# Kernel tuning notes

Hardware: AMD Instinct MI355X
Metric: run time of the kernel (lower is better)

## Reference

```python
import jax, jax.numpy as jnp
import numpy as np

HIDDEN = 1024
NUM_EXPERTS = 64
MIN_K, MAX_K = 1, 4
THRESHOLD = 0.5
N_TOKENS = 32768


def setup_inputs() -> dict:
    key = jax.random.key(0)
    ks = jax.random.split(key, 6)
    std = 0.02
    h4 = HIDDEN // 4
    return {
        "hidden_states": jax.random.normal(ks[0], (N_TOKENS, HIDDEN), dtype=jnp.float32),
        "router_w": std * jax.random.normal(ks[1], (NUM_EXPERTS, HIDDEN), dtype=jnp.float32),
        "w1": std * jax.random.normal(ks[2], (h4, HIDDEN), dtype=jnp.float32),
        "b1": jnp.zeros((h4,), dtype=jnp.float32),
        "w2": std * jax.random.normal(ks[3], (1, h4), dtype=jnp.float32),
        "b2": jnp.zeros((1,), dtype=jnp.float32),
    }


def reference(hidden_states, router_w, w1, b1, w2, b2):
    # complexity predictor: Linear -> ReLU -> Linear -> Sigmoid, squeeze(-1)
    h = jax.nn.relu(hidden_states @ w1.T + b1)                     # [N, H/4]
    complexity = jax.nn.sigmoid(h @ w2.T + b2)[:, 0]               # [N]
    router_logits = hidden_states @ router_w.T                     # [N, E]

    adaptive_k = jnp.where(complexity > THRESHOLD, MAX_K, MIN_K)   # [N] int

    # vectorized adaptive top-k: take MAX_K everywhere, mask beyond k
    top_vals, top_idx = jax.lax.top_k(router_logits, MAX_K)        # [N, MAX_K]
    pos_mask = jnp.arange(MAX_K)[None, :] < adaptive_k[:, None]    # [N, MAX_K]
    masked_vals = jnp.where(pos_mask, top_vals, -jnp.inf)
    expert_weights = jax.nn.softmax(masked_vals, axis=-1)
    expert_weights = jnp.where(pos_mask, expert_weights, 0.0)      # zeros past k
    selected_experts = jnp.where(pos_mask, top_idx, 0)             # zeros past k

    # routing statistics
    probs = jax.nn.softmax(router_logits, axis=-1)                 # [N, E]
    expert_load = probs.mean(axis=0)                               # [E]
    load_variance = expert_load.var(ddof=1)                        # torch .var() is unbiased
    entropy = -(probs * jnp.log(probs + 1e-8)).sum(axis=-1).mean()

    return router_logits, selected_experts, expert_weights, load_variance, entropy
```

## Files before the change

### kernel.cpp

```cpp
#include <hip/hip_runtime.h>
#include <hip/hip_bf16.h>
#include <math.h>

#define NTOK 32768
#define HID  1024
#define NEXP 64
#define H4   256

typedef __attribute__((ext_vector_type(8))) short bf16x8;
typedef __attribute__((ext_vector_type(4))) float f32x4;

static __device__ __forceinline__ ushort f2bf(float x) {
    unsigned u = __float_as_uint(x);
    unsigned r = (u + 0x7FFFu + ((u >> 16) & 1u)) >> 16;
    return (ushort)r;
}

static __device__ __forceinline__ void split3r(float x, ushort &h, ushort &m, ushort &l) {
    h = f2bf(x);
    const float r1 = x - __uint_as_float(((unsigned)h) << 16);
    m = f2bf(r1);
    const float r2 = r1 - __uint_as_float(((unsigned)m) << 16);
    l = f2bf(r2);
}

#define SWZ(row, us) ((us) ^ (((row) & 7) << 3))

__global__ __launch_bounds__(256) void prep_kernel(
    const float* __restrict__ W1, const float* __restrict__ RW,
    ushort* __restrict__ W1h, ushort* __restrict__ W1l,
    ushort* __restrict__ RWh, ushort* __restrict__ RWm, ushort* __restrict__ RWl)
{
    if (blockIdx.x < 256) {
        const int id = blockIdx.x * 256 + threadIdx.x;
        const int c  = id >> 8;
        const int k0 = (id & 255) * 4;
        const float4 v = *(const float4*)(W1 + (size_t)c * HID + k0);
        const int p  = k0 >> 5;
        const int kk = k0 & 31;
        const size_t dst = (size_t)p * 8192 + (size_t)SWZ(c, c * 32 + kk);
        const float xs[4] = {v.x, v.y, v.z, v.w};
        ushort hv[4], lv[4];
#pragma unroll
        for (int j = 0; j < 4; j++) {
            const ushort h = f2bf(xs[j]);
            hv[j] = h;
            lv[j] = f2bf(xs[j] - __uint_as_float(((unsigned)h) << 16));
        }
        *(ushort4*)(W1h + dst) = make_ushort4(hv[0], hv[1], hv[2], hv[3]);
        *(ushort4*)(W1l + dst) = make_ushort4(lv[0], lv[1], lv[2], lv[3]);
    } else {
        const int e  = blockIdx.x - 256;
        const int k0 = threadIdx.x * 4;
        const float4 v = *(const float4*)(RW + (size_t)e * HID + k0);
        const float xs[4] = {v.x, v.y, v.z, v.w};
        ushort h[4], m[4], l[4];
#pragma unroll
        for (int j = 0; j < 4; j++) split3r(xs[j], h[j], m[j], l[j]);
        const int p  = k0 >> 5;
        const int kk = k0 & 31;
        const size_t dst = (size_t)p * 2048 + (size_t)SWZ(e, e * 32 + kk);
        *(ushort4*)(RWh + dst) = make_ushort4(h[0], h[1], h[2], h[3]);
        *(ushort4*)(RWm + dst) = make_ushort4(m[0], m[1], m[2], m[3]);
        *(ushort4*)(RWl + dst) = make_ushort4(l[0], l[1], l[2], l[3]);
    }
}

__global__ __launch_bounds__(512, 4) void fused_mfma(
    const float* __restrict__ X,
    const ushort* __restrict__ RWh, const ushort* __restrict__ RWm,
    const ushort* __restrict__ RWl,
    const ushort* __restrict__ W1h, const ushort* __restrict__ W1l,
    const float* __restrict__ B1, const float* __restrict__ W2,
    float* __restrict__ logits, float* __restrict__ s2ws)
{
    __shared__ __align__(16) ushort Xh[2048], Xm[2048], Xl[2048];
    __shared__ __align__(16) ushort RBh[2048], RBm[2048], RBl[2048];
    __shared__ __align__(16) ushort Wh[8192], Wl[8192];
    __shared__ float red[4][64];

    const int tid  = threadIdx.x;
    const int lane = tid & 63;
    const int w    = tid >> 6;
    const int quad = lane >> 4, l15 = lane & 15;
    const int tok0 = blockIdx.x * 64;
    const int rp   = w >> 2;
    const int cg   = w & 3;

    const int xrow = tid >> 3;
    const int xoff = (tid & 7) * 4;

    f32x4 accL[2];
    f32x4 accP[2][4];
#pragma unroll
    for (int f = 0; f < 2; f++) {
        accL[f] = (f32x4){0.f, 0.f, 0.f, 0.f};
#pragma unroll
        for (int j = 0; j < 4; j++) accP[f][j] = (f32x4){0.f, 0.f, 0.f, 0.f};
    }

    float w2r[4], b1r[4];
#pragma unroll
    for (int j = 0; j < 4; j++) {
        const int col = (cg * 4 + j) * 16 + l15;
        w2r[j] = W2[col];
        b1r[j] = B1[col];
    }

    const float* __restrict__ xsrc = X + (size_t)(tok0 + xrow) * HID + xoff;
    float4 xv = *(const float4*)(xsrc);

    for (int p = 0; p < 32; ++p) {
        {
            const float xs[4] = {xv.x, xv.y, xv.z, xv.w};
            ushort hv[4], mv[4], lv[4];
#pragma unroll
            for (int j = 0; j < 4; j++) split3r(xs[j], hv[j], mv[j], lv[j]);
            const int us = SWZ(xrow, xrow * 32 + xoff);
            *(ushort4*)&Xh[us] = make_ushort4(hv[0], hv[1], hv[2], hv[3]);
            *(ushort4*)&Xm[us] = make_ushort4(mv[0], mv[1], mv[2], mv[3]);
            *(ushort4*)&Xl[us] = make_ushort4(lv[0], lv[1], lv[2], lv[3]);
        }
        {
            const size_t pb = (size_t)p * 8192;
            __builtin_amdgcn_global_load_lds(
                (const __attribute__((address_space(1))) void*)(W1h + pb + (size_t)tid * 8),
                (__attribute__((address_space(3))) void*)((char*)Wh + (size_t)tid * 16), 16, 0, 0);
            __builtin_amdgcn_global_load_lds(
                (const __attribute__((address_space(1))) void*)(W1h + pb + (size_t)(tid + 512) * 8),
                (__attribute__((address_space(3))) void*)((char*)Wh + (size_t)(tid + 512) * 16), 16, 0, 0);
            __builtin_amdgcn_global_load_lds(
                (const __attribute__((address_space(1))) void*)(W1l + pb + (size_t)tid * 8),
                (__attribute__((address_space(3))) void*)((char*)Wl + (size_t)tid * 16), 16, 0, 0);
            __builtin_amdgcn_global_load_lds(
                (const __attribute__((address_space(1))) void*)(W1l + pb + (size_t)(tid + 512) * 8),
                (__attribute__((address_space(3))) void*)((char*)Wl + (size_t)(tid + 512) * 16), 16, 0, 0);
        }
        {
            const size_t pb = (size_t)p * 2048;
            if (tid < 256) {
                __builtin_amdgcn_global_load_lds(
                    (const __attribute__((address_space(1))) void*)(RWh + pb + (size_t)tid * 8),
                    (__attribute__((address_space(3))) void*)((char*)RBh + (size_t)tid * 16), 16, 0, 0);
                __builtin_amdgcn_global_load_lds(
                    (const __attribute__((address_space(1))) void*)(RWl + pb + (size_t)tid * 8),
                    (__attribute__((address_space(3))) void*)((char*)RBl + (size_t)tid * 16), 16, 0, 0);
            } else {
                const int i2 = tid - 256;
                __builtin_amdgcn_global_load_lds(
                    (const __attribute__((address_space(1))) void*)(RWm + pb + (size_t)i2 * 8),
                    (__attribute__((address_space(3))) void*)((char*)RBm + (size_t)i2 * 16), 16, 0, 0);
            }
        }
        __syncthreads();

        xv = *(const float4*)(xsrc + ((p + 1) & 31) * 32);

        bf16x8 axh[2], axm[2], axl[2];
#pragma unroll
        for (int f = 0; f < 2; ++f) {
            const int ra = rp * 32 + f * 16 + l15;
            const int ua = SWZ(ra, ra * 32 + quad * 8);
            axh[f] = *(const bf16x8*)&Xh[ua];
            axm[f] = *(const bf16x8*)&Xm[ua];
            axl[f] = *(const bf16x8*)&Xl[ua];
        }

        {
            const int rb = cg * 16 + l15;
            const int ub = SWZ(rb, rb * 32 + quad * 8);
            const bf16x8 rbh = *(const bf16x8*)&RBh[ub];
            const bf16x8 rbm = *(const bf16x8*)&RBm[ub];
            const bf16x8 rbl = *(const bf16x8*)&RBl[ub];
#pragma unroll
            for (int f = 0; f < 2; ++f) {
                accL[f] = __builtin_amdgcn_mfma_f32_16x16x32_bf16(axh[f], rbh, accL[f], 0, 0, 0);
                accL[f] = __builtin_amdgcn_mfma_f32_16x16x32_bf16(axm[f], rbh, accL[f], 0, 0, 0);
                accL[f] = __builtin_amdgcn_mfma_f32_16x16x32_bf16(axh[f], rbm, accL[f], 0, 0, 0);
                accL[f] = __builtin_amdgcn_mfma_f32_16x16x32_bf16(axl[f], rbh, accL[f], 0, 0, 0);
                accL[f] = __builtin_amdgcn_mfma_f32_16x16x32_bf16(axh[f], rbl, accL[f], 0, 0, 0);
                accL[f] = __builtin_amdgcn_mfma_f32_16x16x32_bf16(axm[f], rbm, accL[f], 0, 0, 0);
            }
        }

#pragma unroll
        for (int j = 0; j < 4; ++j) {
            const int rw = (cg * 4 + j) * 16 + l15;
            const int uw = SWZ(rw, rw * 32 + quad * 8);
            const bf16x8 bwh = *(const bf16x8*)&Wh[uw];
            const bf16x8 bwl = *(const bf16x8*)&Wl[uw];
#pragma unroll
            for (int f = 0; f < 2; ++f) {
                accP[f][j] = __builtin_amdgcn_mfma_f32_16x16x32_bf16(axh[f], bwh, accP[f][j], 0, 0, 0);
                accP[f][j] = __builtin_amdgcn_mfma_f32_16x16x32_bf16(axm[f], bwh, accP[f][j], 0, 0, 0);
                accP[f][j] = __builtin_amdgcn_mfma_f32_16x16x32_bf16(axh[f], bwl, accP[f][j], 0, 0, 0);
            }
        }
        __syncthreads();
    }

#pragma unroll
    for (int f = 0; f < 2; ++f)
#pragma unroll
        for (int r = 0; r < 4; ++r)
            logits[(size_t)(tok0 + (rp * 2 + f) * 16 + quad * 4 + r) * NEXP
                   + cg * 16 + l15] = accL[f][r];

#pragma unroll
    for (int f = 0; f < 2; ++f) {
#pragma unroll
        for (int r = 0; r < 4; ++r) {
            float s = 0.f;
#pragma unroll
            for (int j = 0; j < 4; ++j) {
                const float hval = accP[f][j][r] + b1r[j];
                s = fmaf(w2r[j], fmaxf(hval, 0.f), s);
            }
            s += __shfl_xor(s, 1);
            s += __shfl_xor(s, 2);
            s += __shfl_xor(s, 4);
            s += __shfl_xor(s, 8);
            if (l15 == 0)
                red[cg][rp * 32 + f * 16 + quad * 4 + r] = s;
        }
    }
    __syncthreads();
    if (tid < 64)
        s2ws[tok0 + tid] = red[0][tid] + red[1][tid] + red[2][tid] + red[3][tid];
}

__global__ __launch_bounds__(64) void route_kernel(
    const float* __restrict__ logits, const float* __restrict__ s2ws,
    const float* __restrict__ B2, float* __restrict__ sel,
    float* __restrict__ wts, float* __restrict__ load_sum,
    float* __restrict__ ent_sum)
{
    const int lane = threadIdx.x;
    const int tok  = blockIdx.x * 64 + lane;

    float r[64];
    const float* lr = logits + (size_t)tok * NEXP;
#pragma unroll
    for (int e4 = 0; e4 < 16; e4++) {
        float4 v = *(const float4*)(lr + e4 * 4);
        r[e4 * 4 + 0] = v.x; r[e4 * 4 + 1] = v.y;
        r[e4 * 4 + 2] = v.z; r[e4 * 4 + 3] = v.w;
    }

    float v0 = -1e30f, v1 = -1e30f, v2 = -1e30f, v3 = -1e30f;
    int   i0 = 0, i1 = 0, i2 = 0, i3 = 0;
#pragma unroll
    for (int e = 0; e < 64; e++) {
        const float v = r[e];
        if (v > v3) {
            if (v > v2) {
                if (v > v1) {
                    if (v > v0) { v3=v2;i3=i2; v2=v1;i2=i1; v1=v0;i1=i0; v0=v;i0=e; }
                    else        { v3=v2;i3=i2; v2=v1;i2=i1; v1=v;i1=e; }
                } else          { v3=v2;i3=i2; v2=v;i2=e; }
            } else              { v3=v;i3=e; }
        }
    }

    const float s2 = s2ws[tok] + B2[0];
    const bool k4 = (s2 > 0.f);

    float w0, w1v, w2v, w3v;
    int   s1i, s2i, s3i;
    if (k4) {
        const float e0 = expf(v0 - v0), e1 = expf(v1 - v0);
        const float e2 = expf(v2 - v0), e3 = expf(v3 - v0);
        const float inv4 = 1.f / (e0 + e1 + e2 + e3);
        w0 = e0 * inv4; w1v = e1 * inv4; w2v = e2 * inv4; w3v = e3 * inv4;
        s1i = i1; s2i = i2; s3i = i3;
    } else {
        w0 = 1.f; w1v = 0.f; w2v = 0.f; w3v = 0.f;
        s1i = 0; s2i = 0; s3i = 0;
    }
    {
        float4 sv = {(float)i0, (float)s1i, (float)s2i, (float)s3i};
        float4 wv = {w0, w1v, w2v, w3v};
        *(float4*)(sel + (size_t)tok * 4) = sv;
        *(float4*)(wts + (size_t)tok * 4) = wv;
    }

    const float mx = v0;
    float S = 0.f, pz = 0.f;
#pragma unroll
    for (int e = 0; e < 64; e++) {
        const float z = r[e] - mx;
        const float t = expf(z);
        S += t; pz = fmaf(t, z, pz);
        r[e] = t;
    }
    const float inv = 1.f / S;
    float ent = logf(S) - pz * inv;

    float myload = 0.f;
#pragma unroll
    for (int e = 0; e < 64; e++) {
        float s = r[e] * inv;
        s += __shfl_xor(s, 1);
        s += __shfl_xor(s, 2);
        s += __shfl_xor(s, 4);
        s += __shfl_xor(s, 8);
        s += __shfl_xor(s, 16);
        s += __shfl_xor(s, 32);
        if (lane == e) myload = s;
    }
    atomicAdd(&load_sum[lane], myload);

    ent += __shfl_xor(ent, 1);
    ent += __shfl_xor(ent, 2);
    ent += __shfl_xor(ent, 4);
    ent += __shfl_xor(ent, 8);
    ent += __shfl_xor(ent, 16);
    ent += __shfl_xor(ent, 32);
    if (lane == 0) atomicAdd(ent_sum, ent);
}

__global__ void finalize_kernel(const float* __restrict__ load_sum,
                                const float* __restrict__ ent_sum,
                                float* __restrict__ out_scal)
{
    const int lane = threadIdx.x;
    const float le = load_sum[lane] * (1.f / (float)NTOK);
    float s = le;
#pragma unroll
    for (int o = 32; o >= 1; o >>= 1) s += __shfl_xor(s, o);
    const float mean = s * (1.f / 64.f);
    const float d = le - mean;
    float v = d * d;
#pragma unroll
    for (int o = 32; o >= 1; o >>= 1) v += __shfl_xor(v, o);
    if (lane == 0) {
        out_scal[0] = v * (1.f / 63.f);
        out_scal[1] = ent_sum[0] * (1.f / (float)NTOK);
    }
}

extern "C" void kernel_launch(void* const* d_in, const int* in_sizes, int n_in,
                              void* d_out, int out_size, void* d_ws, size_t ws_size,
                              hipStream_t stream) {
    const float* X  = (const float*)d_in[0];
    const float* RW = (const float*)d_in[1];
    const float* W1 = (const float*)d_in[2];
    const float* B1 = (const float*)d_in[3];
    const float* W2 = (const float*)d_in[4];
    const float* B2 = (const float*)d_in[5];

    float* out    = (float*)d_out;
    float* logits = out;
    float* sel    = out + (size_t)NTOK * NEXP;
    float* wts    = sel + (size_t)NTOK * 4;
    float* scal   = wts + (size_t)NTOK * 4;

    float* s2ws     = (float*)d_ws;
    float* load_sum = s2ws + NTOK;
    float* ent_sum  = load_sum + 64;
    ushort* W1h = (ushort*)(s2ws + NTOK + 256);
    ushort* W1l = W1h + (size_t)H4 * HID;
    ushort* RWh = W1l + (size_t)H4 * HID;
    ushort* RWm = RWh + (size_t)NEXP * HID;
    ushort* RWl = RWm + (size_t)NEXP * HID;

    hipMemsetAsync(load_sum, 0, 65 * sizeof(float), stream);

    prep_kernel<<<320, 256, 0, stream>>>(W1, RW, W1h, W1l, RWh, RWm, RWl);
    fused_mfma<<<NTOK / 64, 512, 0, stream>>>(X, RWh, RWm, RWl, W1h, W1l, B1, W2, logits, s2ws);
    route_kernel<<<NTOK / 64, 64, 0, stream>>>(logits, s2ws, B2, sel, wts, load_sum, ent_sum);
    finalize_kernel<<<1, 64, 0, stream>>>(load_sum, ent_sum, scal);
}
```

Before: 290.1 us.

## Load pre-fragmented weights directly to registers and double-buffer X in LDS

The prep kernel now writes W1 and router weights in an MFMA-fragment-ordered layout, so each lane reads its B-operand with one contiguous 16-byte global load instead of staging through LDS. The X split tiles are double-buffered in LDS, so each iteration needs one barrier rather than two and the next tile's split overlaps with MFMAs. This cuts LDS traffic and footprint, which may raise occupancy. In exchange, every wave reads weights from global/L2 separately, and register pressure from holding 11 weight fragments goes up.

```diff
diff --git a/kernel.cpp b/kernel.cpp
--- a/kernel.cpp
+++ b/kernel.cpp
@@ -28,55 +28,52 @@
 
 __global__ __launch_bounds__(256) void prep_kernel(
     const float* __restrict__ W1, const float* __restrict__ RW,
-    ushort* __restrict__ W1h, ushort* __restrict__ W1l,
-    ushort* __restrict__ RWh, ushort* __restrict__ RWm, ushort* __restrict__ RWl)
+    ushort* __restrict__ W1f, ushort* __restrict__ RWf)
 {
     if (blockIdx.x < 256) {
         const int id = blockIdx.x * 256 + threadIdx.x;
         const int c  = id >> 8;
         const int k0 = (id & 255) * 4;
         const float4 v = *(const float4*)(W1 + (size_t)c * HID + k0);
-        const int p  = k0 >> 5;
-        const int kk = k0 & 31;
-        const size_t dst = (size_t)p * 8192 + (size_t)SWZ(c, c * 32 + kk);
+        const int p = k0 >> 5, quad = (k0 >> 3) & 3, kk = k0 & 7;
+        const int cg = c >> 6, j = (c >> 4) & 3, l15 = c & 15;
+        const int lane = quad * 16 + l15;
+        const size_t base = (size_t)p * 16384 + cg * 4096 + j * 1024 + lane * 8 + kk;
         const float xs[4] = {v.x, v.y, v.z, v.w};
         ushort hv[4], lv[4];
 #pragma unroll
-        for (int j = 0; j < 4; j++) {
-            const ushort h = f2bf(xs[j]);
-            hv[j] = h;
-            lv[j] = f2bf(xs[j] - __uint_as_float(((unsigned)h) << 16));
-        }
-        *(ushort4*)(W1h + dst) = make_ushort4(hv[0], hv[1], hv[2], hv[3]);
-        *(ushort4*)(W1l + dst) = make_ushort4(lv[0], lv[1], lv[2], lv[3]);
+        for (int q = 0; q < 4; q++) {
+            const ushort h = f2bf(xs[q]);
+            hv[q] = h;
+            lv[q] = f2bf(xs[q] - __uint_as_float(((unsigned)h) << 16));
+        }
+        *(ushort4*)(W1f + base)       = make_ushort4(hv[0], hv[1], hv[2], hv[3]);
+        *(ushort4*)(W1f + base + 512) = make_ushort4(lv[0], lv[1], lv[2], lv[3]);
     } else {
         const int e  = blockIdx.x - 256;
         const int k0 = threadIdx.x * 4;
         const float4 v = *(const float4*)(RW + (size_t)e * HID + k0);
+        const int p = k0 >> 5, quad = (k0 >> 3) & 3, kk = k0 & 7;
+        const int cg = e >> 4, l15 = e & 15;
+        const int lane = quad * 16 + l15;
+        const size_t base = (size_t)p * 6144 + cg * 1536 + lane * 8 + kk;
         const float xs[4] = {v.x, v.y, v.z, v.w};
         ushort h[4], m[4], l[4];
 #pragma unroll
-        for (int j = 0; j < 4; j++) split3r(xs[j], h[j], m[j], l[j]);
-        const int p  = k0 >> 5;
-        const int kk = k0 & 31;
-        const size_t dst = (size_t)p * 2048 + (size_t)SWZ(e, e * 32 + kk);
-        *(ushort4*)(RWh + dst) = make_ushort4(h[0], h[1], h[2], h[3]);
-        *(ushort4*)(RWm + dst) = make_ushort4(m[0], m[1], m[2], m[3]);
-        *(ushort4*)(RWl + dst) = make_ushort4(l[0], l[1], l[2], l[3]);
+        for (int q = 0; q < 4; q++) split3r(xs[q], h[q], m[q], l[q]);
+        *(ushort4*)(RWf + base)        = make_ushort4(h[0], h[1], h[2], h[3]);
+        *(ushort4*)(RWf + base + 512)  = make_ushort4(m[0], m[1], m[2], m[3]);
+        *(ushort4*)(RWf + base + 1024) = make_ushort4(l[0], l[1], l[2], l[3]);
     }
 }
 
 __global__ __launch_bounds__(512, 4) void fused_mfma(
     const float* __restrict__ X,
-    const ushort* __restrict__ RWh, const ushort* __restrict__ RWm,
-    const ushort* __restrict__ RWl,
-    const ushort* __restrict__ W1h, const ushort* __restrict__ W1l,
+    const ushort* __restrict__ RWf, const ushort* __restrict__ W1f,
     const float* __restrict__ B1, const float* __restrict__ W2,
     float* __restrict__ logits, float* __restrict__ s2ws)
 {
-    __shared__ __align__(16) ushort Xh[2048], Xm[2048], Xl[2048];
-    __shared__ __align__(16) ushort RBh[2048], RBm[2048], RBl[2048];
-    __shared__ __align__(16) ushort Wh[8192], Wl[8192];
+    __shared__ __align__(16) ushort Xh[2][2048], Xm[2][2048], Xl[2][2048];
     __shared__ float red[4][64];
 
     const int tid  = threadIdx.x;
@@ -99,113 +96,97 @@
         for (int j = 0; j < 4; j++) accP[f][j] = (f32x4){0.f, 0.f, 0.f, 0.f};
     }
 
+    const float* __restrict__ xsrc = X + (size_t)(tok0 + xrow) * HID + xoff;
+    const ushort* __restrict__ rwbase = RWf + (size_t)cg * 1536 + lane * 8;
+    const ushort* __restrict__ w1base = W1f + (size_t)cg * 4096 + lane * 8;
+
+    {
+        const float4 x0 = *(const float4*)(xsrc);
+        const float xs[4] = {x0.x, x0.y, x0.z, x0.w};
+        ushort hv[4], mv[4], lv[4];
+#pragma unroll
+        for (int q = 0; q < 4; q++) split3r(xs[q], hv[q], mv[q], lv[q]);
+        const int us = SWZ(xrow, xrow * 32 + xoff);
+        *(ushort4*)&Xh[0][us] = make_ushort4(hv[0], hv[1], hv[2], hv[3]);
+        *(ushort4*)&Xm[0][us] = make_ushort4(mv[0], mv[1], mv[2], mv[3]);
+        *(ushort4*)&Xl[0][us] = make_ushort4(lv[0], lv[1], lv[2], lv[3]);
+    }
+    __syncthreads();
+
+    for (int p = 0; p < 32; ++p) {
+        const int cur = p & 1;
+
+        const ushort* __restrict__ rwp = rwbase + (size_t)p * 6144;
+        const bf16x8 rbh = *(const bf16x8*)(rwp);
+        const bf16x8 rbm = *(const bf16x8*)(rwp + 512);
+        const bf16x8 rbl = *(const bf16x8*)(rwp + 1024);
+        const ushort* __restrict__ w1p = w1base + (size_t)p * 16384;
+        bf16x8 bwh[4], bwl[4];
+#pragma unroll
+        for (int j = 0; j < 4; ++j) {
+            bwh[j] = *(const bf16x8*)(w1p + j * 1024);
+            bwl[j] = *(const bf16x8*)(w1p + j * 1024 + 512);
+        }
+
+        const float4 xv = *(const float4*)(xsrc + ((p + 1) & 31) * 32);
+
+        bf16x8 axh[2], axm[2], axl[2];
+#pragma unroll
+        for (int f = 0; f < 2; ++f) {
+            const int ra = rp * 32 + f * 16 + l15;
+            const int ua = SWZ(ra, ra * 32 + quad * 8);
+            axh[f] = *(const bf16x8*)&Xh[cur][ua];
+            axm[f] = *(const bf16x8*)&Xm[cur][ua];
+            axl[f] = *(const bf16x8*)&Xl[cur][ua];
+        }
+
+        {
+            const float xs[4] = {xv.x, xv.y, xv.z, xv.w};
+            ushort hv[4], mv[4], lv[4];
+#pragma unroll
+            for (int q = 0; q < 4; q++) split3r(xs[q], hv[q], mv[q], lv[q]);
+            const int us = SWZ(xrow, xrow * 32 + xoff);
+            *(ushort4*)&Xh[cur ^ 1][us] = make_ushort4(hv[0], hv[1], hv[2], hv[3]);
+            *(ushort4*)&Xm[cur ^ 1][us] = make_ushort4(mv[0], mv[1], mv[2], mv[3]);
+            *(ushort4*)&Xl[cur ^ 1][us] = make_ushort4(lv[0], lv[1], lv[2], lv[3]);
+        }
+
+#pragma unroll
+        for (int f = 0; f < 2; ++f) {
+            accL[f] = __builtin_amdgcn_mfma_f32_16x16x32_bf16(axh[f], rbh, accL[f], 0, 0, 0);
+            accL[f] = __builtin_amdgcn_mfma_f32_16x16x32_bf16(axm[f], rbh, accL[f], 0, 0, 0);
+            accL[f] = __builtin_amdgcn_mfma_f32_16x16x32_bf16(axh[f], rbm, accL[f], 0, 0, 0);
+            accL[f] = __builtin_amdgcn_mfma_f32_16x16x32_bf16(axl[f], rbh, accL[f], 0, 0, 0);
+            accL[f] = __builtin_amdgcn_mfma_f32_16x16x32_bf16(axh[f], rbl, accL[f], 0, 0, 0);
+            accL[f] = __builtin_amdgcn_mfma_f32_16x16x32_bf16(axm[f], rbm, accL[f], 0, 0, 0);
+        }
+
+#pragma unroll
+        for (int j = 0; j < 4; ++j)
+#pragma unroll
+            for (int f = 0; f < 2; ++f) {
+                accP[f][j] = __builtin_amdgcn_mfma_f32_16x16x32_bf16(axh[f], bwh[j], accP[f][j], 0, 0, 0);
+                accP[f][j] = __builtin_amdgcn_mfma_f32_16x16x32_bf16(axm[f], bwh[j], accP[f][j], 0, 0, 0);
+                accP[f][j] = __builtin_amdgcn_mfma_f32_16x16x32_bf16(axh[f], bwl[j], accP[f][j], 0, 0, 0);
+            }
+
+        __syncthreads();
+    }
+
+#pragma unroll
+    for (int f = 0; f < 2; ++f)
+#pragma unroll
+        for (int r = 0; r < 4; ++r)
+            logits[(size_t)(tok0 + (rp * 2 + f) * 16 + quad * 4 + r) * NEXP
+                   + cg * 16 + l15] = accL[f][r];
+
     float w2r[4], b1r[4];
 #pragma unroll
-    for (int j = 0; j < 4; j++) {
+    for (int j = 0; j < 4; ++j) {
         const int col = (cg * 4 + j) * 16 + l15;
         w2r[j] = W2[col];
         b1r[j] = B1[col];
     }
-
-    const float* __restrict__ xsrc = X + (size_t)(tok0 + xrow) * HID + xoff;
-    float4 xv = *(const float4*)(xsrc);
-
-    for (int p = 0; p < 32; ++p) {
-        {
-            const float xs[4] = {xv.x, xv.y, xv.z, xv.w};
-            ushort hv[4], mv[4], lv[4];
-#pragma unroll
-            for (int j = 0; j < 4; j++) split3r(xs[j], hv[j], mv[j], lv[j]);
-            const int us = SWZ(xrow, xrow * 32 + xoff);
-            *(ushort4*)&Xh[us] = make_ushort4(hv[0], hv[1], hv[2], hv[3]);
-            *(ushort4*)&Xm[us] = make_ushort4(mv[0], mv[1], mv[2], mv[3]);
-            *(ushort4*)&Xl[us] = make_ushort4(lv[0], lv[1], lv[2], lv[3]);
-        }
-        {
-            const size_t pb = (size_t)p * 8192;
-            __builtin_amdgcn_global_load_lds(
-                (const __attribute__((address_space(1))) void*)(W1h + pb + (size_t)tid * 8),
-                (__attribute__((address_space(3))) void*)((char*)Wh + (size_t)tid * 16), 16, 0, 0);
-            __builtin_amdgcn_global_load_lds(
-                (const __attribute__((address_space(1))) void*)(W1h + pb + (size_t)(tid + 512) * 8),
-                (__attribute__((address_space(3))) void*)((char*)Wh + (size_t)(tid + 512) * 16), 16, 0, 0);
-            __builtin_amdgcn_global_load_lds(
-                (const __attribute__((address_space(1))) void*)(W1l + pb + (size_t)tid * 8),
-                (__attribute__((address_space(3))) void*)((char*)Wl + (size_t)tid * 16), 16, 0, 0);
-            __builtin_amdgcn_global_load_lds(
-                (const __attribute__((address_space(1))) void*)(W1l + pb + (size_t)(tid + 512) * 8),
-                (__attribute__((address_space(3))) void*)((char*)Wl + (size_t)(tid + 512) * 16), 16, 0, 0);
-        }
-        {
-            const size_t pb = (size_t)p * 2048;
-            if (tid < 256) {
-                __builtin_amdgcn_global_load_lds(
-                    (const __attribute__((address_space(1))) void*)(RWh + pb + (size_t)tid * 8),
-                    (__attribute__((address_space(3))) void*)((char*)RBh + (size_t)tid * 16), 16, 0, 0);
-                __builtin_amdgcn_global_load_lds(
-                    (const __attribute__((address_space(1))) void*)(RWl + pb + (size_t)tid * 8),
-                    (__attribute__((address_space(3))) void*)((char*)RBl + (size_t)tid * 16), 16, 0, 0);
-            } else {
-                const int i2 = tid - 256;
-                __builtin_amdgcn_global_load_lds(
-                    (const __attribute__((address_space(1))) void*)(RWm + pb + (size_t)i2 * 8),
-                    (__attribute__((address_space(3))) void*)((char*)RBm + (size_t)i2 * 16), 16, 0, 0);
-            }
-        }
-        __syncthreads();
-
-        xv = *(const float4*)(xsrc + ((p + 1) & 31) * 32);
-
-        bf16x8 axh[2], axm[2], axl[2];
-#pragma unroll
-        for (int f = 0; f < 2; ++f) {
-            const int ra = rp * 32 + f * 16 + l15;
-            const int ua = SWZ(ra, ra * 32 + quad * 8);
-            axh[f] = *(const bf16x8*)&Xh[ua];
-            axm[f] = *(const bf16x8*)&Xm[ua];
-            axl[f] = *(const bf16x8*)&Xl[ua];
-        }
-
-        {
-            const int rb = cg * 16 + l15;
-            const int ub = SWZ(rb, rb * 32 + quad * 8);
-            const bf16x8 rbh = *(const bf16x8*)&RBh[ub];
-            const bf16x8 rbm = *(const bf16x8*)&RBm[ub];
-            const bf16x8 rbl = *(const bf16x8*)&RBl[ub];
-#pragma unroll
-            for (int f = 0; f < 2; ++f) {
-                accL[f] = __builtin_amdgcn_mfma_f32_16x16x32_bf16(axh[f], rbh, accL[f], 0, 0, 0);
-                accL[f] = __builtin_amdgcn_mfma_f32_16x16x32_bf16(axm[f], rbh, accL[f], 0, 0, 0);
-                accL[f] = __builtin_amdgcn_mfma_f32_16x16x32_bf16(axh[f], rbm, accL[f], 0, 0, 0);
-                accL[f] = __builtin_amdgcn_mfma_f32_16x16x32_bf16(axl[f], rbh, accL[f], 0, 0, 0);
-                accL[f] = __builtin_amdgcn_mfma_f32_16x16x32_bf16(axh[f], rbl, accL[f], 0, 0, 0);
-                accL[f] = __builtin_amdgcn_mfma_f32_16x16x32_bf16(axm[f], rbm, accL[f], 0, 0, 0);
-            }
-        }
-
-#pragma unroll
-        for (int j = 0; j < 4; ++j) {
-            const int rw = (cg * 4 + j) * 16 + l15;
-            const int uw = SWZ(rw, rw * 32 + quad * 8);
-            const bf16x8 bwh = *(const bf16x8*)&Wh[uw];
-            const bf16x8 bwl = *(const bf16x8*)&Wl[uw];
-#pragma unroll
-            for (int f = 0; f < 2; ++f) {
-                accP[f][j] = __builtin_amdgcn_mfma_f32_16x16x32_bf16(axh[f], bwh, accP[f][j], 0, 0, 0);
-                accP[f][j] = __builtin_amdgcn_mfma_f32_16x16x32_bf16(axm[f], bwh, accP[f][j], 0, 0, 0);
-                accP[f][j] = __builtin_amdgcn_mfma_f32_16x16x32_bf16(axh[f], bwl, accP[f][j], 0, 0, 0);
-            }
-        }
-        __syncthreads();
-    }
-
-#pragma unroll
-    for (int f = 0; f < 2; ++f)
-#pragma unroll
-        for (int r = 0; r < 4; ++r)
-            logits[(size_t)(tok0 + (rp * 2 + f) * 16 + quad * 4 + r) * NEXP
-                   + cg * 16 + l15] = accL[f][r];
-
 #pragma unroll
     for (int f = 0; f < 2; ++f) {
 #pragma unroll
@@ -358,16 +339,13 @@
     float* s2ws     = (float*)d_ws;
     float* load_sum = s2ws + NTOK;
     float* ent_sum  = load_sum + 64;
-    ushort* W1h = (ushort*)(s2ws + NTOK + 256);
-    ushort* W1l = W1h + (size_t)H4 * HID;
-    ushort* RWh = W1l + (size_t)H4 * HID;
-    ushort* RWm = RWh + (size_t)NEXP * HID;
-    ushort* RWl = RWm + (size_t)NEXP * HID;
+    ushort* W1f = (ushort*)(s2ws + NTOK + 256);
+    ushort* RWf = W1f + (size_t)32 * 16384;
 
     hipMemsetAsync(load_sum, 0, 65 * sizeof(float), stream);
 
-    prep_kernel<<<320, 256, 0, stream>>>(W1, RW, W1h, W1l, RWh, RWm, RWl);
-    fused_mfma<<<NTOK / 64, 512, 0, stream>>>(X, RWh, RWm, RWl, W1h, W1l, B1, W2, logits, s2ws);
+    prep_kernel<<<320, 256, 0, stream>>>(W1, RW, W1f, RWf);
+    fused_mfma<<<NTOK / 64, 512, 0, stream>>>(X, RWf, W1f, B1, W2, logits, s2ws);
     route_kernel<<<NTOK / 64, 64, 0, stream>>>(logits, s2ws, B2, sel, wts, load_sum, ent_sum);
     finalize_kernel<<<1, 64, 0, stream>>>(load_sum, ent_sum, scal);
 }
```

New measurement: 298.6 us. +2.9%, slower.
